# Kernel tuning notes

Hardware: AMD Instinct MI355X
Metric: run time of the kernel (lower is better)

## Reference

```python
import jax, jax.numpy as jnp
import numpy as np

S = 1e-05
BLOCK = 8


def _dct_mat():
    # D[k, n] = dct_coeff(k, n, 8); basis[u,v,x,y] = D[u,x]*D[v,y]
    n = np.arange(BLOCK)
    k = np.arange(BLOCK)[:, None]
    D = np.sqrt(2.0 / BLOCK) * np.cos(np.pi * k * (2 * n + 1) / (2 * BLOCK))
    D[0, :] = np.sqrt(1.0 / BLOCK)
    return jnp.asarray(D, dtype=jnp.float32)


def setup_inputs() -> dict:
    key = jax.random.key(0)
    k1, k2, k3 = jax.random.split(key, 3)
    # 8-bit-range pixels, as the JPEG math (chroma +128 offset, clamp 255) assumes
    x = jax.random.uniform(k1, (128, 3, 256, 256), dtype=jnp.float32) * 255.0
    q_luminance = jax.random.uniform(k2, (8, 8), dtype=jnp.float32, minval=S, maxval=2 * S)
    q_chrominance = jax.random.uniform(k3, (8, 8), dtype=jnp.float32, minval=S, maxval=2 * S)
    return {"x": x, "q_luminance": q_luminance, "q_chrominance": q_chrominance}


def reference(x, q_luminance, q_chrominance):
    D = _dct_mat()
    B, C, H, W = x.shape  # C == 3, H == W == 256 (hardcoded in original module)
    r, g, b = x[:, 0], x[:, 1], x[:, 2]

    # RGB -> YCbCr (JPEG constants, +128 chroma offset)
    y = 0.299 * r + 0.587 * g + 0.114 * b
    cb = -0.168736 * r - 0.331264 * g + 0.5 * b + 128.0
    cr = 0.5 * r - 0.418688 * g - 0.081312 * b + 128.0

    nh, nw = H // BLOCK, W // BLOCK

    def to_blocks(c):  # [B,H,W] -> [B,nh,nw,8,8]
        return c.reshape(B, nh, BLOCK, nw, BLOCK).transpose(0, 1, 3, 2, 4)

    def dct(c):  # separable 8x8 DCT: basis[u,v,m,n] = D[u,m]*D[v,n]
        return jnp.einsum('bijmn,um,vn->bijuv', to_blocks(c), D, D)

    def idct(c):  # [B,nh,nw,8,8] coeffs -> [B,H,W] pixels
        blocks = jnp.einsum('bijuv,um,vn->bijmn', c, D, D)
        return blocks.transpose(0, 1, 3, 2, 4).reshape(B, H, W)

    def quant_dequant(c, q):
        qs = q / S  # effective table ~ Uniform(1, 2)
        return jnp.round(c / qs) * qs

    y_rec = idct(quant_dequant(dct(y), q_luminance))
    cb_rec = idct(quant_dequant(dct(cb), q_chrominance)) - 128.0
    cr_rec = idct(quant_dequant(dct(cr), q_chrominance)) - 128.0

    # YCbCr -> RGB exactly as in the original (note: blue row uses 1.722 * Cb,
    # faithfully reproducing the source code's constants)
    r2 = y_rec + 1.402 * cr_rec
    g2 = y_rec - 0.344136 * cb_rec - 0.714136 * cr_rec
    b2 = y_rec + 1.722 * cb_rec

    return jnp.clip(jnp.stack([r2, g2, b2], axis=1), 0.0, 255.0)
```

## Files before the change

### kernel.cpp

```cpp
#include <hip/hip_runtime.h>
#include <math.h>

static constexpr float Dm[8][8] = {
  { 0.3535533906f, 0.3535533906f, 0.3535533906f, 0.3535533906f, 0.3535533906f, 0.3535533906f, 0.3535533906f, 0.3535533906f},
  { 0.4903926402f, 0.4157348062f, 0.2777851165f, 0.0975451610f,-0.0975451610f,-0.2777851165f,-0.4157348062f,-0.4903926402f},
  { 0.4619397663f, 0.1913417162f,-0.1913417162f,-0.4619397663f,-0.4619397663f,-0.1913417162f, 0.1913417162f, 0.4619397663f},
  { 0.4157348062f,-0.0975451610f,-0.4903926402f,-0.2777851165f, 0.2777851165f, 0.4903926402f, 0.0975451610f,-0.4157348062f},
  { 0.3535533906f,-0.3535533906f,-0.3535533906f, 0.3535533906f, 0.3535533906f,-0.3535533906f,-0.3535533906f, 0.3535533906f},
  { 0.2777851165f,-0.4903926402f, 0.0975451610f, 0.4157348062f,-0.4157348062f,-0.0975451610f, 0.4903926402f,-0.2777851165f},
  { 0.1913417162f,-0.4619397663f, 0.4619397663f,-0.1913417162f,-0.1913417162f, 0.4619397663f,-0.4619397663f, 0.1913417162f},
  { 0.0975451610f,-0.2777851165f, 0.4157348062f,-0.4903926402f, 0.4903926402f,-0.4157348062f, 0.2777851165f,-0.0975451610f},
};

#define PLS 257
#define SBS 72

__global__ __launch_bounds__(256) void jpeg_fused(
    const float* __restrict__ x,
    const float* __restrict__ qlum,
    const float* __restrict__ qchr,
    float* __restrict__ out)
{
  __shared__ float plane[3][8 * PLS];
  __shared__ float scr[32 * SBS];
  __shared__ float qq[2][64];

  const int t  = threadIdx.x;
  const int wg = blockIdx.x;
  const int bb = wg >> 5;
  const int br = wg & 31;
  const int base = bb * (3 * 65536) + br * (8 * 256);

  if (t < 64)            qq[0][t]      = qlum[t]      / 1e-5f;
  else if (t < 128)      qq[1][t - 64] = qchr[t - 64] / 1e-5f;

  {
    const float* rp = x + base;
    const float* gp = rp + 65536;
    const float* bp = gp + 65536;
#pragma unroll
    for (int k = 0; k < 8; ++k) {
      float r = rp[k * 256 + t];
      float g = gp[k * 256 + t];
      float b = bp[k * 256 + t];
      plane[0][k * PLS + t] =  0.299f   * r + 0.587f    * g + 0.114f    * b;
      plane[1][k * PLS + t] = -0.168736f* r - 0.331264f * g + 0.5f      * b + 128.0f;
      plane[2][k * PLS + t] =  0.5f     * r - 0.418688f * g - 0.081312f * b + 128.0f;
    }
  }
  __syncthreads();

  const int b8 = t >> 3;
  const int r8 = t & 7;
  const int sb = b8 * SBS;

#pragma unroll 1
  for (int ch = 0; ch < 3; ++ch) {
    {
      float xr[8];
#pragma unroll
      for (int m = 0; m < 8; ++m) xr[m] = plane[ch][r8 * PLS + b8 * 8 + m];
#pragma unroll
      for (int v = 0; v < 8; ++v) {
        float acc = xr[0] * Dm[v][0];
#pragma unroll
        for (int m = 1; m < 8; ++m) acc = fmaf(xr[m], Dm[v][m], acc);
        scr[sb + v * 9 + r8] = acc;
      }
    }
    __syncthreads();

    float Z[8];
    {
      float tc[8];
#pragma unroll
      for (int r = 0; r < 8; ++r) tc[r] = scr[sb + r8 * 9 + r];
      const float* qp = qq[(ch == 0) ? 0 : 1];
      float Fv[8];
#pragma unroll
      for (int u = 0; u < 8; ++u) {
        float acc = tc[0] * Dm[u][0];
#pragma unroll
        for (int r = 1; r < 8; ++r) acc = fmaf(tc[r], Dm[u][r], acc);
        float q = qp[u * 8 + r8];
        Fv[u] = rintf(acc / q) * q;
      }
#pragma unroll
      for (int m = 0; m < 8; ++m) {
        float acc = Fv[0] * Dm[0][m];
#pragma unroll
        for (int u = 1; u < 8; ++u) acc = fmaf(Fv[u], Dm[u][m], acc);
        Z[m] = acc;
      }
    }
    __syncthreads();
#pragma unroll
    for (int m = 0; m < 8; ++m) scr[sb + m * 9 + r8] = Z[m];
    __syncthreads();

    {
      float zr[8];
#pragma unroll
      for (int v = 0; v < 8; ++v) zr[v] = scr[sb + r8 * 9 + v];
#pragma unroll
      for (int j = 0; j < 8; ++j) {
        float acc = zr[0] * Dm[0][j];
#pragma unroll
        for (int v = 1; v < 8; ++v) acc = fmaf(zr[v], Dm[v][j], acc);
        plane[ch][r8 * PLS + b8 * 8 + j] = acc;
      }
    }
    __syncthreads();
  }

  {
    float* orp = out + base;
    float* ogp = orp + 65536;
    float* obp = ogp + 65536;
#pragma unroll
    for (int k = 0; k < 8; ++k) {
      float y  = plane[0][k * PLS + t];
      float cb = plane[1][k * PLS + t] - 128.0f;
      float cr = plane[2][k * PLS + t] - 128.0f;
      float r2 = fmaf( 1.402f, cr, y);
      float g2 = y - 0.344136f * cb - 0.714136f * cr;
      float b2 = fmaf( 1.722f, cb, y);
      orp[k * 256 + t] = fminf(fmaxf(r2, 0.0f), 255.0f);
      ogp[k * 256 + t] = fminf(fmaxf(g2, 0.0f), 255.0f);
      obp[k * 256 + t] = fminf(fmaxf(b2, 0.0f), 255.0f);
    }
  }
}

extern "C" void kernel_launch(void* const* d_in, const int* in_sizes, int n_in,
                              void* d_out, int out_size, void* d_ws, size_t ws_size,
                              hipStream_t stream) {
  (void)in_sizes; (void)n_in; (void)out_size; (void)d_ws; (void)ws_size;
  const float* x    = (const float*)d_in[0];
  const float* qlum = (const float*)d_in[1];
  const float* qchr = (const float*)d_in[2];
  float* out = (float*)d_out;
  jpeg_fused<<<dim3(4096), dim3(256), 0, stream>>>(x, qlum, qchr, out);
}
```

Measured before the change: 180.7 us.

## Partition work per wavefront, replace block barriers with wave-local sync, vectorize I/O

Each 64-lane wavefront now owns a 64-column slice of the 8-row strip with its own shared-memory plane and scratch, so every __syncthreads is replaced by an lgkmcnt wait plus a scheduling barrier. Global loads and stores and the LDS accesses become float4. The quantization tables are held in registers, and the division is replaced by multiplication with a precomputed reciprocal. The aim is to remove block-wide barrier stalls and scalar memory ops. The risks are LDS bank conflicts with the new padding, extra registers, and rounding differences from multiplying by the reciprocal instead of dividing.

```diff
diff --git a/kernel.cpp b/kernel.cpp
--- a/kernel.cpp
+++ b/kernel.cpp
@@ -12,8 +12,15 @@
   { 0.0975451610f,-0.2777851165f, 0.4157348062f,-0.4903926402f, 0.4903926402f,-0.4157348062f, 0.2777851165f,-0.0975451610f},
 };
 
-#define PLS 257
-#define SBS 72
+#define ROWS    68
+#define PL_CH   (8 * ROWS)
+#define PL_WAVE (3 * PL_CH)
+#define SCR_BLK 68
+#define SCR_WAVE (8 * SCR_BLK)
+
+#define WAVE_SYNC() do { \
+  asm volatile("s_waitcnt lgkmcnt(0)" ::: "memory"); \
+  __builtin_amdgcn_sched_barrier(0); } while (0)
 
 __global__ __launch_bounds__(256) void jpeg_fused(
     const float* __restrict__ x,
@@ -21,114 +28,150 @@
     const float* __restrict__ qchr,
     float* __restrict__ out)
 {
-  __shared__ float plane[3][8 * PLS];
-  __shared__ float scr[32 * SBS];
-  __shared__ float qq[2][64];
+  __shared__ __attribute__((aligned(16))) float plane[4 * PL_WAVE];
+  __shared__ __attribute__((aligned(16))) float scr[4 * SCR_WAVE];
 
   const int t  = threadIdx.x;
+  const int w  = t >> 6;
+  const int l  = t & 63;
   const int wg = blockIdx.x;
   const int bb = wg >> 5;
   const int br = wg & 31;
   const int base = bb * (3 * 65536) + br * (8 * 256);
 
-  if (t < 64)            qq[0][t]      = qlum[t]      / 1e-5f;
-  else if (t < 128)      qq[1][t - 64] = qchr[t - 64] / 1e-5f;
+  const int colg = (w << 6) + ((l & 15) << 2);
+  const int r0   = l >> 4;
+  const int b8l  = l >> 3;
+  const int r8   = l & 7;
 
-  {
-    const float* rp = x + base;
-    const float* gp = rp + 65536;
-    const float* bp = gp + 65536;
+  float* pw = &plane[w * PL_WAVE];
+  float* sw = &scr[w * SCR_WAVE];
+
+  float qsl[8], rql[8], qsc[8], rqc[8];
 #pragma unroll
-    for (int k = 0; k < 8; ++k) {
-      float r = rp[k * 256 + t];
-      float g = gp[k * 256 + t];
-      float b = bp[k * 256 + t];
-      plane[0][k * PLS + t] =  0.299f   * r + 0.587f    * g + 0.114f    * b;
-      plane[1][k * PLS + t] = -0.168736f* r - 0.331264f * g + 0.5f      * b + 128.0f;
-      plane[2][k * PLS + t] =  0.5f     * r - 0.418688f * g - 0.081312f * b + 128.0f;
-    }
+  for (int u = 0; u < 8; ++u) {
+    qsl[u] = qlum[u * 8 + r8] / 1e-5f;  rql[u] = 1.0f / qsl[u];
+    qsc[u] = qchr[u * 8 + r8] / 1e-5f;  rqc[u] = 1.0f / qsc[u];
   }
-  __syncthreads();
 
-  const int b8 = t >> 3;
-  const int r8 = t & 7;
-  const int sb = b8 * SBS;
+#pragma unroll
+  for (int rg = 0; rg < 2; ++rg) {
+    const int row = r0 + 4 * rg;
+    const float* px = x + base + row * 256 + colg;
+    float4 r = *(const float4*)(px);
+    float4 g = *(const float4*)(px + 65536);
+    float4 b = *(const float4*)(px + 131072);
+    float4 y, cb, cr;
+    y.x  =  0.299f*r.x + 0.587f*g.x + 0.114f*b.x;
+    y.y  =  0.299f*r.y + 0.587f*g.y + 0.114f*b.y;
+    y.z  =  0.299f*r.z + 0.587f*g.z + 0.114f*b.z;
+    y.w  =  0.299f*r.w + 0.587f*g.w + 0.114f*b.w;
+    cb.x = -0.168736f*r.x - 0.331264f*g.x + 0.5f*b.x + 128.0f;
+    cb.y = -0.168736f*r.y - 0.331264f*g.y + 0.5f*b.y + 128.0f;
+    cb.z = -0.168736f*r.z - 0.331264f*g.z + 0.5f*b.z + 128.0f;
+    cb.w = -0.168736f*r.w - 0.331264f*g.w + 0.5f*b.w + 128.0f;
+    cr.x =  0.5f*r.x - 0.418688f*g.x - 0.081312f*b.x + 128.0f;
+    cr.y =  0.5f*r.y - 0.418688f*g.y - 0.081312f*b.y + 128.0f;
+    cr.z =  0.5f*r.z - 0.418688f*g.z - 0.081312f*b.z + 128.0f;
+    cr.w =  0.5f*r.w - 0.418688f*g.w - 0.081312f*b.w + 128.0f;
+    const int pidx = row * ROWS + ((l & 15) << 2);
+    *(float4*)&pw[0 * PL_CH + pidx] = y;
+    *(float4*)&pw[1 * PL_CH + pidx] = cb;
+    *(float4*)&pw[2 * PL_CH + pidx] = cr;
+  }
+  WAVE_SYNC();
 
-#pragma unroll 1
+#pragma unroll
   for (int ch = 0; ch < 3; ++ch) {
+    float* prow = &pw[ch * PL_CH + r8 * ROWS + 8 * b8l];
+    float* scol = &sw[b8l * SCR_BLK + 8 * r8];
+
     {
-      float xr[8];
-#pragma unroll
-      for (int m = 0; m < 8; ++m) xr[m] = plane[ch][r8 * PLS + b8 * 8 + m];
+      float4 x0 = *(const float4*)&prow[0];
+      float4 x1 = *(const float4*)&prow[4];
+      float xr[8] = {x0.x,x0.y,x0.z,x0.w,x1.x,x1.y,x1.z,x1.w};
 #pragma unroll
       for (int v = 0; v < 8; ++v) {
         float acc = xr[0] * Dm[v][0];
 #pragma unroll
         for (int m = 1; m < 8; ++m) acc = fmaf(xr[m], Dm[v][m], acc);
-        scr[sb + v * 9 + r8] = acc;
+        sw[b8l * SCR_BLK + 8 * v + r8] = acc;
       }
     }
-    __syncthreads();
+    WAVE_SYNC();
 
-    float Z[8];
     {
-      float tc[8];
-#pragma unroll
-      for (int r = 0; r < 8; ++r) tc[r] = scr[sb + r8 * 9 + r];
-      const float* qp = qq[(ch == 0) ? 0 : 1];
+      float4 t0 = *(const float4*)&scol[0];
+      float4 t1 = *(const float4*)&scol[4];
+      float tc[8] = {t0.x,t0.y,t0.z,t0.w,t1.x,t1.y,t1.z,t1.w};
       float Fv[8];
 #pragma unroll
       for (int u = 0; u < 8; ++u) {
         float acc = tc[0] * Dm[u][0];
 #pragma unroll
         for (int r = 1; r < 8; ++r) acc = fmaf(tc[r], Dm[u][r], acc);
-        float q = qp[u * 8 + r8];
-        Fv[u] = rintf(acc / q) * q;
+        const float qu = (ch == 0) ? qsl[u] : qsc[u];
+        const float ru = (ch == 0) ? rql[u] : rqc[u];
+        Fv[u] = rintf(acc * ru) * qu;
       }
 #pragma unroll
       for (int m = 0; m < 8; ++m) {
         float acc = Fv[0] * Dm[0][m];
 #pragma unroll
         for (int u = 1; u < 8; ++u) acc = fmaf(Fv[u], Dm[u][m], acc);
-        Z[m] = acc;
+        sw[b8l * SCR_BLK + 8 * m + r8] = acc;
       }
     }
-    __syncthreads();
-#pragma unroll
-    for (int m = 0; m < 8; ++m) scr[sb + m * 9 + r8] = Z[m];
-    __syncthreads();
+    WAVE_SYNC();
 
     {
-      float zr[8];
-#pragma unroll
-      for (int v = 0; v < 8; ++v) zr[v] = scr[sb + r8 * 9 + v];
+      float4 z0 = *(const float4*)&scol[0];
+      float4 z1 = *(const float4*)&scol[4];
+      float zr[8] = {z0.x,z0.y,z0.z,z0.w,z1.x,z1.y,z1.z,z1.w};
+      float yj[8];
 #pragma unroll
       for (int j = 0; j < 8; ++j) {
         float acc = zr[0] * Dm[0][j];
 #pragma unroll
         for (int v = 1; v < 8; ++v) acc = fmaf(zr[v], Dm[v][j], acc);
-        plane[ch][r8 * PLS + b8 * 8 + j] = acc;
+        yj[j] = acc;
       }
+      float4 y0 = {yj[0], yj[1], yj[2], yj[3]};
+      float4 y1 = {yj[4], yj[5], yj[6], yj[7]};
+      *(float4*)&prow[0] = y0;
+      *(float4*)&prow[4] = y1;
     }
-    __syncthreads();
   }
+  WAVE_SYNC();
 
-  {
-    float* orp = out + base;
-    float* ogp = orp + 65536;
-    float* obp = ogp + 65536;
 #pragma unroll
-    for (int k = 0; k < 8; ++k) {
-      float y  = plane[0][k * PLS + t];
-      float cb = plane[1][k * PLS + t] - 128.0f;
-      float cr = plane[2][k * PLS + t] - 128.0f;
-      float r2 = fmaf( 1.402f, cr, y);
-      float g2 = y - 0.344136f * cb - 0.714136f * cr;
-      float b2 = fmaf( 1.722f, cb, y);
-      orp[k * 256 + t] = fminf(fmaxf(r2, 0.0f), 255.0f);
-      ogp[k * 256 + t] = fminf(fmaxf(g2, 0.0f), 255.0f);
-      obp[k * 256 + t] = fminf(fmaxf(b2, 0.0f), 255.0f);
-    }
+  for (int rg = 0; rg < 2; ++rg) {
+    const int row = r0 + 4 * rg;
+    const int pidx = row * ROWS + ((l & 15) << 2);
+    float4 y  = *(const float4*)&pw[0 * PL_CH + pidx];
+    float4 cb = *(const float4*)&pw[1 * PL_CH + pidx];
+    float4 cr = *(const float4*)&pw[2 * PL_CH + pidx];
+    cb.x -= 128.0f; cb.y -= 128.0f; cb.z -= 128.0f; cb.w -= 128.0f;
+    cr.x -= 128.0f; cr.y -= 128.0f; cr.z -= 128.0f; cr.w -= 128.0f;
+    float4 rr, gg, bbv;
+    rr.x = fmaf(1.402f, cr.x, y.x);  rr.y = fmaf(1.402f, cr.y, y.y);
+    rr.z = fmaf(1.402f, cr.z, y.z);  rr.w = fmaf(1.402f, cr.w, y.w);
+    gg.x = y.x - 0.344136f*cb.x - 0.714136f*cr.x;
+    gg.y = y.y - 0.344136f*cb.y - 0.714136f*cr.y;
+    gg.z = y.z - 0.344136f*cb.z - 0.714136f*cr.z;
+    gg.w = y.w - 0.344136f*cb.w - 0.714136f*cr.w;
+    bbv.x = fmaf(1.722f, cb.x, y.x); bbv.y = fmaf(1.722f, cb.y, y.y);
+    bbv.z = fmaf(1.722f, cb.z, y.z); bbv.w = fmaf(1.722f, cb.w, y.w);
+    rr.x = fminf(fmaxf(rr.x, 0.0f), 255.0f);  rr.y = fminf(fmaxf(rr.y, 0.0f), 255.0f);
+    rr.z = fminf(fmaxf(rr.z, 0.0f), 255.0f);  rr.w = fminf(fmaxf(rr.w, 0.0f), 255.0f);
+    gg.x = fminf(fmaxf(gg.x, 0.0f), 255.0f);  gg.y = fminf(fmaxf(gg.y, 0.0f), 255.0f);
+    gg.z = fminf(fmaxf(gg.z, 0.0f), 255.0f);  gg.w = fminf(fmaxf(gg.w, 0.0f), 255.0f);
+    bbv.x = fminf(fmaxf(bbv.x, 0.0f), 255.0f); bbv.y = fminf(fmaxf(bbv.y, 0.0f), 255.0f);
+    bbv.z = fminf(fmaxf(bbv.z, 0.0f), 255.0f); bbv.w = fminf(fmaxf(bbv.w, 0.0f), 255.0f);
+    float* po = out + base + row * 256 + colg;
+    *(float4*)(po)          = rr;
+    *(float4*)(po + 65536)  = gg;
+    *(float4*)(po + 131072) = bbv;
   }
 }
 
```

Result: no change. 181.9 us (+0.6%).

## Restructure JPEG kernel to per-thread rows with wave-local LDS and float4 IO

Applied to the files above, without the earlier changes.

Each thread now loads one 8-pixel block row per channel straight into registers with float4 loads, does the color conversion and first DCT pass in registers, and uses a small per-wave LDS scratch for the transposes. Block-wide __syncthreads are replaced by wave-local waitcnt barriers, and the three channels are processed back to back without a channel loop. Quant division becomes multiplication by a precomputed reciprocal, and the q tables are loaded per thread. This aims to cut LDS traffic, block barriers and uncoalesced plane staging. The reciprocal multiply may round differently from true division at quantization ties.

```diff
diff --git a/kernel.cpp b/kernel.cpp
--- a/kernel.cpp
+++ b/kernel.cpp
@@ -12,8 +12,13 @@
   { 0.0975451610f,-0.2777851165f, 0.4157348062f,-0.4903926402f, 0.4903926402f,-0.4157348062f, 0.2777851165f,-0.0975451610f},
 };
 
-#define PLS 257
-#define SBS 72
+#define SCR_BLK 68
+#define SCR_CH  (8 * SCR_BLK)
+#define SCR_WAVE (3 * SCR_CH)
+
+#define WAVE_SYNC() do { \
+  asm volatile("s_waitcnt lgkmcnt(0)" ::: "memory"); \
+  __builtin_amdgcn_sched_barrier(0); } while (0)
 
 __global__ __launch_bounds__(256) void jpeg_fused(
     const float* __restrict__ x,
@@ -21,115 +26,125 @@
     const float* __restrict__ qchr,
     float* __restrict__ out)
 {
-  __shared__ float plane[3][8 * PLS];
-  __shared__ float scr[32 * SBS];
-  __shared__ float qq[2][64];
+  __shared__ __attribute__((aligned(16))) float scr[4 * SCR_WAVE];
 
   const int t  = threadIdx.x;
+  const int w  = t >> 6;
+  const int l  = t & 63;
   const int wg = blockIdx.x;
   const int bb = wg >> 5;
   const int br = wg & 31;
-  const int base = bb * (3 * 65536) + br * (8 * 256);
 
-  if (t < 64)            qq[0][t]      = qlum[t]      / 1e-5f;
-  else if (t < 128)      qq[1][t - 64] = qchr[t - 64] / 1e-5f;
+  const int blk = l >> 3;
+  const int r8  = l & 7;
+  const int goff = bb * (3 * 65536) + br * (8 * 256) + r8 * 256 + (w * 8 + blk) * 8;
 
-  {
-    const float* rp = x + base;
-    const float* gp = rp + 65536;
-    const float* bp = gp + 65536;
+  float* sw = &scr[w * SCR_WAVE];
+  float* sb0 = &sw[0 * SCR_CH + blk * SCR_BLK];
+  float* sb1 = &sw[1 * SCR_CH + blk * SCR_BLK];
+  float* sb2 = &sw[2 * SCR_CH + blk * SCR_BLK];
+
+  const float* px = x + goff;
+  float4 R0 = *(const float4*)(px);
+  float4 R1 = *(const float4*)(px + 4);
+  float4 G0 = *(const float4*)(px + 65536);
+  float4 G1 = *(const float4*)(px + 65540);
+  float4 B0 = *(const float4*)(px + 131072);
+  float4 B1 = *(const float4*)(px + 131076);
+
+  float qsl[8], rql[8], qsc[8], rqc[8];
 #pragma unroll
-    for (int k = 0; k < 8; ++k) {
-      float r = rp[k * 256 + t];
-      float g = gp[k * 256 + t];
-      float b = bp[k * 256 + t];
-      plane[0][k * PLS + t] =  0.299f   * r + 0.587f    * g + 0.114f    * b;
-      plane[1][k * PLS + t] = -0.168736f* r - 0.331264f * g + 0.5f      * b + 128.0f;
-      plane[2][k * PLS + t] =  0.5f     * r - 0.418688f * g - 0.081312f * b + 128.0f;
-    }
-  }
-  __syncthreads();
-
-  const int b8 = t >> 3;
-  const int r8 = t & 7;
-  const int sb = b8 * SBS;
-
-#pragma unroll 1
-  for (int ch = 0; ch < 3; ++ch) {
-    {
-      float xr[8];
-#pragma unroll
-      for (int m = 0; m < 8; ++m) xr[m] = plane[ch][r8 * PLS + b8 * 8 + m];
-#pragma unroll
-      for (int v = 0; v < 8; ++v) {
-        float acc = xr[0] * Dm[v][0];
-#pragma unroll
-        for (int m = 1; m < 8; ++m) acc = fmaf(xr[m], Dm[v][m], acc);
-        scr[sb + v * 9 + r8] = acc;
-      }
-    }
-    __syncthreads();
-
-    float Z[8];
-    {
-      float tc[8];
-#pragma unroll
-      for (int r = 0; r < 8; ++r) tc[r] = scr[sb + r8 * 9 + r];
-      const float* qp = qq[(ch == 0) ? 0 : 1];
-      float Fv[8];
-#pragma unroll
-      for (int u = 0; u < 8; ++u) {
-        float acc = tc[0] * Dm[u][0];
-#pragma unroll
-        for (int r = 1; r < 8; ++r) acc = fmaf(tc[r], Dm[u][r], acc);
-        float q = qp[u * 8 + r8];
-        Fv[u] = rintf(acc / q) * q;
-      }
-#pragma unroll
-      for (int m = 0; m < 8; ++m) {
-        float acc = Fv[0] * Dm[0][m];
-#pragma unroll
-        for (int u = 1; u < 8; ++u) acc = fmaf(Fv[u], Dm[u][m], acc);
-        Z[m] = acc;
-      }
-    }
-    __syncthreads();
-#pragma unroll
-    for (int m = 0; m < 8; ++m) scr[sb + m * 9 + r8] = Z[m];
-    __syncthreads();
-
-    {
-      float zr[8];
-#pragma unroll
-      for (int v = 0; v < 8; ++v) zr[v] = scr[sb + r8 * 9 + v];
-#pragma unroll
-      for (int j = 0; j < 8; ++j) {
-        float acc = zr[0] * Dm[0][j];
-#pragma unroll
-        for (int v = 1; v < 8; ++v) acc = fmaf(zr[v], Dm[v][j], acc);
-        plane[ch][r8 * PLS + b8 * 8 + j] = acc;
-      }
-    }
-    __syncthreads();
+  for (int u = 0; u < 8; ++u) {
+    qsl[u] = qlum[u * 8 + r8] / 1e-5f;  rql[u] = 1.0f / qsl[u];
+    qsc[u] = qchr[u * 8 + r8] / 1e-5f;  rqc[u] = 1.0f / qsc[u];
   }
 
-  {
-    float* orp = out + base;
-    float* ogp = orp + 65536;
-    float* obp = ogp + 65536;
+  float rr[8] = {R0.x,R0.y,R0.z,R0.w,R1.x,R1.y,R1.z,R1.w};
+  float gr[8] = {G0.x,G0.y,G0.z,G0.w,G1.x,G1.y,G1.z,G1.w};
+  float brw[8] = {B0.x,B0.y,B0.z,B0.w,B1.x,B1.y,B1.z,B1.w};
+  float yr[8], cbr[8], crr[8];
 #pragma unroll
-    for (int k = 0; k < 8; ++k) {
-      float y  = plane[0][k * PLS + t];
-      float cb = plane[1][k * PLS + t] - 128.0f;
-      float cr = plane[2][k * PLS + t] - 128.0f;
-      float r2 = fmaf( 1.402f, cr, y);
-      float g2 = y - 0.344136f * cb - 0.714136f * cr;
-      float b2 = fmaf( 1.722f, cb, y);
-      orp[k * 256 + t] = fminf(fmaxf(r2, 0.0f), 255.0f);
-      ogp[k * 256 + t] = fminf(fmaxf(g2, 0.0f), 255.0f);
-      obp[k * 256 + t] = fminf(fmaxf(b2, 0.0f), 255.0f);
-    }
+  for (int n = 0; n < 8; ++n) {
+    yr[n]  =  0.299f   * rr[n] + 0.587f    * gr[n] + 0.114f    * brw[n];
+    cbr[n] = -0.168736f* rr[n] - 0.331264f * gr[n] + 0.5f      * brw[n] + 128.0f;
+    crr[n] =  0.5f     * rr[n] - 0.418688f * gr[n] - 0.081312f * brw[n] + 128.0f;
   }
+
+#define PHASE_A(rowarr, sb) do { \
+  _Pragma("unroll") \
+  for (int v = 0; v < 8; ++v) { \
+    float acc = rowarr[0] * Dm[v][0]; \
+    _Pragma("unroll") \
+    for (int m = 1; m < 8; ++m) acc = fmaf(rowarr[m], Dm[v][m], acc); \
+    (sb)[8 * v + r8] = acc; \
+  } } while (0)
+  PHASE_A(yr,  sb0);
+  PHASE_A(cbr, sb1);
+  PHASE_A(crr, sb2);
+#undef PHASE_A
+  WAVE_SYNC();
+
+#define PHASE_B(sb, qs, rq) do { \
+  float4 t0 = *(const float4*)&(sb)[8 * r8]; \
+  float4 t1 = *(const float4*)&(sb)[8 * r8 + 4]; \
+  float tc[8] = {t0.x,t0.y,t0.z,t0.w,t1.x,t1.y,t1.z,t1.w}; \
+  float Fv[8]; \
+  _Pragma("unroll") \
+  for (int u = 0; u < 8; ++u) { \
+    float acc = tc[0] * Dm[u][0]; \
+    _Pragma("unroll") \
+    for (int r = 1; r < 8; ++r) acc = fmaf(tc[r], Dm[u][r], acc); \
+    Fv[u] = rintf(acc * (rq)[u]) * (qs)[u]; \
+  } \
+  _Pragma("unroll") \
+  for (int m = 0; m < 8; ++m) { \
+    float acc = Fv[0] * Dm[0][m]; \
+    _Pragma("unroll") \
+    for (int u = 1; u < 8; ++u) acc = fmaf(Fv[u], Dm[u][m], acc); \
+    (sb)[8 * m + r8] = acc;   \
+  } } while (0)
+  PHASE_B(sb0, qsl, rql);
+  PHASE_B(sb1, qsc, rqc);
+  PHASE_B(sb2, qsc, rqc);
+#undef PHASE_B
+  WAVE_SYNC();
+
+#define PHASE_C(sb, outarr) do { \
+  float4 z0 = *(const float4*)&(sb)[8 * r8]; \
+  float4 z1 = *(const float4*)&(sb)[8 * r8 + 4]; \
+  float zr[8] = {z0.x,z0.y,z0.z,z0.w,z1.x,z1.y,z1.z,z1.w}; \
+  _Pragma("unroll") \
+  for (int j = 0; j < 8; ++j) { \
+    float acc = zr[0] * Dm[0][j]; \
+    _Pragma("unroll") \
+    for (int v = 1; v < 8; ++v) acc = fmaf(zr[v], Dm[v][j], acc); \
+    outarr[j] = acc; \
+  } } while (0)
+  PHASE_C(sb0, yr);
+  PHASE_C(sb1, cbr);
+  PHASE_C(sb2, crr);
+#undef PHASE_C
+
+  float ro[8], go[8], bo[8];
+#pragma unroll
+  for (int j = 0; j < 8; ++j) {
+    float y  = yr[j];
+    float cb = cbr[j] - 128.0f;
+    float cr = crr[j] - 128.0f;
+    float r2 = fmaf(1.402f, cr, y);
+    float g2 = y - 0.344136f * cb - 0.714136f * cr;
+    float b2 = fmaf(1.722f, cb, y);
+    ro[j] = fminf(fmaxf(r2, 0.0f), 255.0f);
+    go[j] = fminf(fmaxf(g2, 0.0f), 255.0f);
+    bo[j] = fminf(fmaxf(b2, 0.0f), 255.0f);
+  }
+  float* po = out + goff;
+  *(float4*)(po)           = (float4){ro[0], ro[1], ro[2], ro[3]};
+  *(float4*)(po + 4)       = (float4){ro[4], ro[5], ro[6], ro[7]};
+  *(float4*)(po + 65536)   = (float4){go[0], go[1], go[2], go[3]};
+  *(float4*)(po + 65540)   = (float4){go[4], go[5], go[6], go[7]};
+  *(float4*)(po + 131072)  = (float4){bo[0], bo[1], bo[2], bo[3]};
+  *(float4*)(po + 131076)  = (float4){bo[4], bo[5], bo[6], bo[7]};
 }
 
 extern "C" void kernel_launch(void* const* d_in, const int* in_sizes, int n_in,
```

Result: no change. 179.9 us (-0.5%).
